# Optimization experiments

Hardware: AMD Instinct MI355X
Metric: run time of the kernel (lower is better)

The kernel has to match this reference:

```python
import jax, jax.numpy as jnp
import numpy as np

N_NODES = 2708      # hardcoded in GCN.__init__ (DictLearn(2708, nfeat/2))
NFEAT = 4096
M_DICT = NFEAT // 2 # dictionary atoms
NHID = 1024
NCLASS = 64
POWER_ITER = 100
FISTA_ITER = 20


def power_method(W, key):
    # nm -> largest eigenvalue of W^T W (sigma_max(W)^2)
    X0 = jax.random.normal(key, (1, W.shape[1]), dtype=W.dtype)
    def body(i, carry):
        X, _ = carry
        Xn = (X @ W.T) @ W
        nm = jnp.linalg.norm(Xn)
        return (Xn / nm, nm)
    _, nm = jax.lax.fori_loop(0, POWER_ITER, body, (X0, jnp.float32(1.0)))
    return nm


def soft_threshold(X, lam):
    return jnp.sign(X) * jax.nn.relu(jnp.abs(X) - lam)


def fista(Y, W, lam, key):
    # torch sets W.requires_grad_(False) during sparse coding
    Ws = jax.lax.stop_gradient(W)
    c = power_method(Ws, key)
    eta = 1.0 / c
    Gamma0 = soft_threshold((eta * Ws).T @ Y, lam)   # (m, nfeat)
    Ynorm = jnp.linalg.norm(Y)
    def step(carry, _):
        Gamma, Z, t = carry
        residual = Ws @ Z - Y                         # (n, nfeat)
        Gamma_new = soft_threshold(Z - eta * (Ws.T @ residual), lam / c)
        t_new = (1.0 + jnp.sqrt(1.0 + 4.0 * t * t)) / 2.0
        Z_new = Gamma_new + (t - 1.0) / t_new * (Gamma_new - Gamma)
        nrm = jnp.linalg.norm(residual) / Ynorm
        return (Gamma_new, Z_new, t_new), nrm
    (Gamma, _, _), norms = jax.lax.scan(
        step, (Gamma0, Gamma0, jnp.float32(1.0)), None, length=FISTA_ITER)
    return Gamma, norms


def setup_inputs() -> dict:
    key = jax.random.key(0)
    ks = jax.random.split(key, 7)
    x = jax.random.normal(ks[0], (N_NODES, NFEAT), dtype=jnp.float32)
    # dense stand-in for the normalized sparse adjacency; scaled to keep activations sane
    adj = jax.random.uniform(ks[1], (N_NODES, N_NODES), dtype=jnp.float32) / N_NODES
    stdv1 = 1.0 / np.sqrt(NHID)
    gc1_w = jax.random.uniform(ks[2], (NFEAT, NHID), minval=-stdv1, maxval=stdv1, dtype=jnp.float32)
    gc1_b = jax.random.uniform(ks[3], (NHID,), minval=-stdv1, maxval=stdv1, dtype=jnp.float32)
    stdv2 = 1.0 / np.sqrt(NCLASS)
    gc2_w = jax.random.uniform(ks[4], (NHID, NCLASS), minval=-stdv2, maxval=stdv2, dtype=jnp.float32)
    gc2_b = jax.random.uniform(ks[5], (NCLASS,), minval=-stdv2, maxval=stdv2, dtype=jnp.float32)
    # torch normalizes W in-place via .data, so the learnable leaf IS the normalized dict
    W_dict = jax.random.normal(ks[6], (N_NODES, M_DICT), dtype=jnp.float32)
    W_dict = W_dict / jnp.linalg.norm(W_dict, axis=0, keepdims=True)
    return {"x": x, "adj": adj, "gc1_w": gc1_w, "gc1_b": gc1_b,
            "gc2_w": gc2_w, "gc2_b": gc2_b, "W_dict": W_dict, "K": 1}


def reference(x, adj, gc1_w, gc1_b, gc2_w, gc2_b, W_dict, K):
    # SC='fista' (the only dimensionally consistent path); K acts as lamda
    lam = jnp.float32(K)
    Gamma, norms = fista(x, W_dict, lam, jax.random.key(1))  # (m, nfeat)
    x_dec = W_dict @ Gamma                                   # (n, nfeat)
    h = jax.nn.relu(adj @ (x_dec @ gc1_w) + gc1_b)           # dropout is identity in eval
    out = adj @ (h @ gc2_w) + gc2_b
    return jax.nn.log_softmax(out, axis=1), x_dec, Gamma, norms
```

## Files before the change

### kernel.cpp

```cpp
#include <hip/hip_runtime.h>
#include <cstdint>
#include <cmath>

#define NN_ 2708
#define NF_ 4096
#define MD_ 2048
#define NH_ 1024
#define NC_ 64
#define FITER 20
#define KPAD 2720


typedef _Float16 half8_t __attribute__((ext_vector_type(8)));
typedef _Float16 half4_t __attribute__((ext_vector_type(4)));
typedef float floatx4_t __attribute__((ext_vector_type(4)));

__device__ __forceinline__ float softt(float v, float t) {
    float a = fabsf(v) - t;
    a = a > 0.f ? a : 0.f;
    return copysignf(a, v);
}

__device__ __forceinline__ float blockReduceSum(float v, float* red) {
    int lane = threadIdx.x & 63, wid = threadIdx.x >> 6;
    #pragma unroll
    for (int off = 32; off; off >>= 1) v += __shfl_down(v, off);
    if (lane == 0) red[wid] = v;
    __syncthreads();
    if (wid == 0) {
        int nw = (blockDim.x + 63) >> 6;
        float r = (lane < nw) ? red[lane] : 0.f;
        #pragma unroll
        for (int off = 4; off; off >>= 1) r += __shfl_down(r, off);
        if (lane == 0) red[0] = r;
    }
    __syncthreads();
    float out = red[0];
    __syncthreads();
    return out;
}

__device__ __forceinline__ float erfinv_f(float x) {
    float w = -log1pf(-x * x);
    float p;
    if (w < 5.0f) {
        w -= 2.5f;
        p = 2.81022636e-08f;
        p = fmaf(p, w, 3.43273939e-07f);
        p = fmaf(p, w, -3.5233877e-06f);
        p = fmaf(p, w, -4.39150654e-06f);
        p = fmaf(p, w, 0.00021858087f);
        p = fmaf(p, w, -0.00125372503f);
        p = fmaf(p, w, -0.00417768164f);
        p = fmaf(p, w, 0.246640727f);
        p = fmaf(p, w, 1.50140941f);
    } else {
        w = sqrtf(w) - 3.0f;
        p = -0.000200214257f;
        p = fmaf(p, w, 0.000100950558f);
        p = fmaf(p, w, 0.00134934322f);
        p = fmaf(p, w, -0.00367342844f);
        p = fmaf(p, w, 0.00573950773f);
        p = fmaf(p, w, -0.0076224613f);
        p = fmaf(p, w, 0.00943887047f);
        p = fmaf(p, w, 1.00167406f);
        p = fmaf(p, w, 2.83297682f);
    }
    return p * x;
}

__device__ __forceinline__ float u32_to_normal(uint32_t bits) {
    uint32_t fb = (bits >> 9) | 0x3F800000u;
    float f = __uint_as_float(fb) - 1.0f;
    const float lo = -0.99999994f;
    float u = fmaf(f, 2.0f, lo);
    u = fmaxf(lo, u);
    return 1.41421356f * erfinv_f(u);
}

__global__ void init_x0_kernel(float* __restrict__ X0) {
    int i = blockIdx.x * blockDim.x + threadIdx.x;
    if (i >= MD_ / 2) return;
    uint32_t x0 = (uint32_t)i, x1 = (uint32_t)(i + MD_ / 2);
    const uint32_t k0 = 0u, k1 = 1u, k2 = 0x1BD11BDBu;
    const uint32_t ks[3] = {k0, k1, k2};
    x0 += k0; x1 += k1;
    const int rot[8] = {13, 15, 26, 6, 17, 29, 16, 24};
    #pragma unroll
    for (int g = 0; g < 5; ++g) {
        const int base = (g & 1) ? 4 : 0;
        #pragma unroll
        for (int rr = 0; rr < 4; ++rr) {
            x0 += x1;
            int r = rot[base + rr];
            x1 = (x1 << r) | (x1 >> (32 - r));
            x1 ^= x0;
        }
        x0 += ks[(g + 1) % 3];
        x1 += ks[(g + 2) % 3] + (uint32_t)(g + 1);
    }
    X0[i] = u32_to_normal(x0);
    X0[i + MD_ / 2] = u32_to_normal(x1);
}

__global__ void zero_scal_kernel(float* __restrict__ scal) {
    int t = threadIdx.x;
    if (t < 32) scal[t] = 0.f;
}

__global__ void fill0_kernel(uint32_t* __restrict__ p, int n32) {
    int i = blockIdx.x * blockDim.x + threadIdx.x;
    if (i < n32) p[i] = 0u;
}

__global__ void sumsq_kernel(const float* __restrict__ X, int n, float* __restrict__ acc) {
    __shared__ float red[8];
    float s = 0.f;
    for (size_t i = (size_t)blockIdx.x * blockDim.x + threadIdx.x; i < (size_t)n;
         i += (size_t)gridDim.x * blockDim.x) {
        float v = X[i];
        s += v * v;
    }
    s = blockReduceSum(s, red);
    if (threadIdx.x == 0) atomicAdd(acc, s);
}

__global__ void tsplit_kernel(const float* __restrict__ src, int R, int ld, int Rpad,
                              _Float16* __restrict__ hi, _Float16* __restrict__ lo) {
    __shared__ float t[32][33];
    int rb = blockIdx.y * 32, cb = blockIdx.x * 32;
    int tx = threadIdx.x & 31, ty = threadIdx.x >> 5;
    #pragma unroll
    for (int s = 0; s < 32; s += 8) {
        int r = rb + ty + s, c = cb + tx;
        t[ty + s][tx] = (r < R) ? src[(size_t)r * ld + c] : 0.f;
    }
    __syncthreads();
    #pragma unroll
    for (int s = 0; s < 32; s += 8) {
        int c = cb + ty + s, r = rb + tx;
        float v = t[tx][ty + s];
        _Float16 h = (_Float16)v;
        size_t o = (size_t)c * Rpad + r;
        hi[o] = h;
        lo[o] = (_Float16)(v - (float)h);
    }
}

__global__ void splitrows_hi_kernel(const float* __restrict__ src, int R, int C,
                                    _Float16* __restrict__ hi) {
    int r = blockIdx.x;
    _Float16* d = hi + (size_t)r * C;
    if (r < R) {
        const float* s = src + (size_t)r * C;
        for (int c = threadIdx.x * 4; c < C; c += 1024) {
            float4 v = *reinterpret_cast<const float4*>(s + c);
            half4_t h;
            h[0] = (_Float16)v.x; h[1] = (_Float16)v.y;
            h[2] = (_Float16)v.z; h[3] = (_Float16)v.w;
            *reinterpret_cast<half4_t*>(d + c) = h;
        }
    } else {
        for (int c = threadIdx.x * 4; c < C; c += 1024) {
            half4_t h = {(_Float16)0.f, (_Float16)0.f, (_Float16)0.f, (_Float16)0.f};
            *reinterpret_cast<half4_t*>(d + c) = h;
        }
    }
}

__global__ void splitadj_hi_kernel(const float* __restrict__ adj, _Float16* __restrict__ hi) {
    int r = blockIdx.x;
    bool rok = r < NN_;
    _Float16* d = hi + (size_t)r * KPAD;
    const float* s = adj + (size_t)r * NN_;
    for (int c = threadIdx.x * 4; c < KPAD; c += 1024) {
        half4_t h = {(_Float16)0.f, (_Float16)0.f, (_Float16)0.f, (_Float16)0.f};
        if (rok && c + 3 < NN_) {
            float4 v = *reinterpret_cast<const float4*>(s + c);
            h[0] = (_Float16)v.x; h[1] = (_Float16)v.y;
            h[2] = (_Float16)v.z; h[3] = (_Float16)v.w;
        }
        *reinterpret_cast<half4_t*>(d + c) = h;
    }
}

__global__ void g0_kernel(const float* __restrict__ Bm, const float* __restrict__ scal,
                          float* __restrict__ Gamma,
                          _Float16* __restrict__ Zh, _Float16* __restrict__ Zl) {
    __shared__ float t[32][33];
    int rb = blockIdx.y * 32;
    int cb = blockIdx.x * 32;
    float eta = scal[1], lam = scal[3];
    int tx = threadIdx.x & 31, ty = threadIdx.x >> 5;
    #pragma unroll
    for (int s = 0; s < 32; s += 8) {
        int r = rb + ty + s, c = cb + tx;
        float g = softt(eta * Bm[(size_t)r * NF_ + c], lam);
        Gamma[(size_t)r * NF_ + c] = g;
        t[ty + s][tx] = g;
    }
    __syncthreads();
    #pragma unroll
    for (int s = 0; s < 32; s += 8) {
        int c = cb + ty + s, r = rb + tx;
        float v = t[tx][ty + s];
        _Float16 h = (_Float16)v;
        size_t o = (size_t)c * MD_ + r;
        Zh[o] = h;
        Zl[o] = (_Float16)(v - (float)h);
    }
}

__global__ __launch_bounds__(256)
void papply_kernel(const _Float16* __restrict__ Mh, const _Float16* __restrict__ Ml,
                   const float* __restrict__ Xc, float* __restrict__ Xn, int addI) {
    __shared__ float xs[MD_];
    __shared__ float red[8];
    const int tid = threadIdx.x;
    float ss = 0.f;
    for (int k = tid; k < MD_; k += 256) { float v = Xc[k]; xs[k] = v; ss += v * v; }
    __syncthreads();
    ss = blockReduceSum(ss, red);
    float inv = 1.0f / sqrtf(ss);
    const int w = tid >> 6, l = tid & 63;
    const int r = blockIdx.x * 4 + w;
    const _Float16* mhr = Mh + (size_t)r * MD_;
    const _Float16* mlr = Ml + (size_t)r * MD_;
    float s = 0.f;
    #pragma unroll
    for (int q = 0; q < 8; ++q) {
        int o = (q * 64 + l) * 4;
        half4_t hv = *reinterpret_cast<const half4_t*>(mhr + o);
        half4_t lv = *reinterpret_cast<const half4_t*>(mlr + o);
        float4 xv = *reinterpret_cast<const float4*>(&xs[o]);
        s = fmaf((float)hv[0] + (float)lv[0], xv.x, s);
        s = fmaf((float)hv[1] + (float)lv[1], xv.y, s);
        s = fmaf((float)hv[2] + (float)lv[2], xv.z, s);
        s = fmaf((float)hv[3] + (float)lv[3], xv.w, s);
    }
    #pragma unroll
    for (int off = 32; off; off >>= 1) s += __shfl_down(s, off);
    if (l == 0) Xn[r] = (s + (addI ? xs[r] : 0.f)) * inv;
}

__global__ void pfinal_kernel(const float* __restrict__ Xf, const int* __restrict__ Kp,
                              float* __restrict__ scal) {
    __shared__ float red[8];
    float ss = 0.f;
    for (int k = threadIdx.x; k < MD_; k += 256) { float v = Xf[k]; ss += v * v; }
    ss = blockReduceSum(ss, red);
    if (threadIdx.x == 0) {
        float c = sqrtf(ss);
        float lam = (float)Kp[0];
        scal[0] = c;
        scal[1] = 1.0f / c;
        scal[2] = lam / c;
        scal[3] = lam;
    }
}

enum { ME_STORE = 0, ME_SYMSPLIT = 1, ME_SYMSPLIT_MI = 2, ME_H1 = 3, ME_SYMSPLIT16 = 4,
       ME_SPLIT_T = 5, ME_FISTAG = 6, ME_FISTAG_LAST = 7, ME_BIAS = 8, ME_BIASRELU = 9 };

__device__ __forceinline__ void stage_h(const _Float16* __restrict__ g, int row0, int K, int kk,
                                        _Float16* s, int tid) {
    const int row = tid >> 2;
    const int kg = (tid & 3) ^ ((row >> 1) & 3);
    const _Float16* gp = g + (size_t)(row0 + row) * K + kk + (kg << 3);
    _Float16* lp = s + ((size_t)((tid >> 6) * 64) << 3);
    __builtin_amdgcn_global_load_lds(
        (const __attribute__((address_space(1))) void*)gp,
        (__attribute__((address_space(3))) void*)lp, 16, 0, 0);
}

template <bool AFP32, bool THREE>
__global__ __launch_bounds__(512)
void mgemm_kernel(const _Float16* __restrict__ Ah, const _Float16* __restrict__ Al,
                  const float* __restrict__ Afp, int Marr,
                  const _Float16* __restrict__ Bh, const _Float16* __restrict__ Bl,
                  int K, int Mvalid, int Nvalid, int ldc,
                  float* __restrict__ C, const float* __restrict__ BmP,
                  const float* __restrict__ bias,
                  _Float16* __restrict__ Th, _Float16* __restrict__ Tl, int Tstride,
                  const float* __restrict__ scal, float betak,
                  float* __restrict__ nrm_acc, int epi) {
    constexpr int TILE = 128 * 32;
    constexpr int TPB = THREE ? 4 : 3;
    constexpr int NT = AFP32 ? 4 : 3 * TPB;
    __shared__ __align__(16) _Float16 smem[NT * TILE];
    float* red = (float*)smem;
    const int tid = threadIdx.x;
    const int w = tid >> 6, l = tid & 63;
    const int wr = w >> 2, wc = w & 3;
    const int quad = l >> 4, lc = l & 15;
    const int row0 = blockIdx.y * 128, col0 = blockIdx.x * 128;

    const int qs = (quad ^ ((lc >> 1) & 3)) << 3;

    floatx4_t acc[4][2];
    #pragma unroll
    for (int i = 0; i < 4; ++i)
        #pragma unroll
        for (int j = 0; j < 2; ++j) {
            floatx4_t z = {0.f, 0.f, 0.f, 0.f};
            acc[i][j] = z;
        }

    if constexpr (!AFP32) {
        const int NTK = K >> 5;
        auto STAGE = [&](int kt, int b) {
            _Float16* base = smem + b * (TPB * TILE);
            stage_h(Ah, row0, K, kt << 5, base, tid);
            if constexpr (THREE) stage_h(Al, row0, K, kt << 5, base + TILE, tid);
            stage_h(Bh, col0, K, kt << 5, base + (THREE ? 2 : 1) * TILE, tid);
            stage_h(Bl, col0, K, kt << 5, base + (THREE ? 3 : 2) * TILE, tid);
        };
        STAGE(0, 0);
        if (NTK > 1) {
            STAGE(1, 1);
            if constexpr (THREE) asm volatile("s_waitcnt vmcnt(4)" ::: "memory");
            else                 asm volatile("s_waitcnt vmcnt(3)" ::: "memory");
        } else {
            asm volatile("s_waitcnt vmcnt(0)" ::: "memory");
        }
        __builtin_amdgcn_s_barrier();
        for (int t = 0; t < NTK; ++t) {
            const int cur = t % 3;
            if (t + 2 < NTK) STAGE(t + 2, (t + 2) % 3);
            const _Float16* base = smem + cur * (TPB * TILE);
            const _Float16* pAh = base;
            const _Float16* pAl = base + TILE;
            const _Float16* pBh = base + (THREE ? 2 : 1) * TILE;
            const _Float16* pBl = base + (THREE ? 3 : 2) * TILE;
            half8_t fAh[4], fAl[4], fBh[2], fBl[2];
            #pragma unroll
            for (int i = 0; i < 4; ++i) {
                int oa = (wr * 64 + i * 16 + lc) * 32 + qs;
                fAh[i] = *reinterpret_cast<const half8_t*>(&pAh[oa]);
                if constexpr (THREE) fAl[i] = *reinterpret_cast<const half8_t*>(&pAl[oa]);
            }
            #pragma unroll
            for (int j = 0; j < 2; ++j) {
                int ob = (wc * 32 + j * 16 + lc) * 32 + qs;
                fBh[j] = *reinterpret_cast<const half8_t*>(&pBh[ob]);
                fBl[j] = *reinterpret_cast<const half8_t*>(&pBl[ob]);
            }
            #pragma unroll
            for (int i = 0; i < 4; ++i)
                #pragma unroll
                for (int j = 0; j < 2; ++j) {
                    acc[i][j] = __builtin_amdgcn_mfma_f32_16x16x32_f16(fAh[i], fBh[j], acc[i][j], 0, 0, 0);
                    acc[i][j] = __builtin_amdgcn_mfma_f32_16x16x32_f16(fAh[i], fBl[j], acc[i][j], 0, 0, 0);
                    if constexpr (THREE)
                        acc[i][j] = __builtin_amdgcn_mfma_f32_16x16x32_f16(fAl[i], fBh[j], acc[i][j], 0, 0, 0);
                }
            __builtin_amdgcn_sched_barrier(0);
            if (t + 2 < NTK) {
                if constexpr (THREE) asm volatile("s_waitcnt vmcnt(4)" ::: "memory");
                else                 asm volatile("s_waitcnt vmcnt(3)" ::: "memory");
            } else {
                asm volatile("s_waitcnt vmcnt(0)" ::: "memory");
            }
            __builtin_amdgcn_s_barrier();
        }
    } else {
        _Float16* sAh = smem;
        _Float16* sAl = smem + TILE;
        _Float16* sBh = smem + 2 * TILE;
        _Float16* sBl = smem + 3 * TILE;
        for (int kk = 0; kk < K; kk += 32) {
            #pragma unroll
            for (int p = 0; p < 2; ++p) {
                int c2 = p * 512 + tid;
                int r2 = c2 >> 3, k4 = (c2 & 7) << 2;
                int gr = row0 + r2;
                gr = gr < Marr ? gr : Marr - 1;
                float4 v = *reinterpret_cast<const float4*>(Afp + (size_t)gr * K + kk + k4);
                half4_t hh, ll;
                hh[0] = (_Float16)v.x; ll[0] = (_Float16)(v.x - (float)hh[0]);
                hh[1] = (_Float16)v.y; ll[1] = (_Float16)(v.y - (float)hh[1]);
                hh[2] = (_Float16)v.z; ll[2] = (_Float16)(v.z - (float)hh[2]);
                hh[3] = (_Float16)v.w; ll[3] = (_Float16)(v.w - (float)hh[3]);
                int sw = (((k4 >> 3) ^ ((r2 >> 1) & 3)) << 3) | (k4 & 7);
                *reinterpret_cast<half4_t*>(&sAh[r2 * 32 + sw]) = hh;
                *reinterpret_cast<half4_t*>(&sAl[r2 * 32 + sw]) = ll;
            }
            stage_h(Bh, col0, K, kk, sBh, tid);
            stage_h(Bl, col0, K, kk, sBl, tid);
            asm volatile("s_waitcnt vmcnt(0)" ::: "memory");
            __syncthreads();

            half8_t fAh[4], fAl[4], fBh[2], fBl[2];
            #pragma unroll
            for (int i = 0; i < 4; ++i) {
                int oa = (wr * 64 + i * 16 + lc) * 32 + qs;
                fAh[i] = *reinterpret_cast<const half8_t*>(&sAh[oa]);
                fAl[i] = *reinterpret_cast<const half8_t*>(&sAl[oa]);
            }
            #pragma unroll
            for (int j = 0; j < 2; ++j) {
                int ob = (wc * 32 + j * 16 + lc) * 32 + qs;
                fBh[j] = *reinterpret_cast<const half8_t*>(&sBh[ob]);
                fBl[j] = *reinterpret_cast<const half8_t*>(&sBl[ob]);
            }
            #pragma unroll
            for (int i = 0; i < 4; ++i)
                #pragma unroll
                for (int j = 0; j < 2; ++j) {
                    acc[i][j] = __builtin_amdgcn_mfma_f32_16x16x32_f16(fAh[i], fBh[j], acc[i][j], 0, 0, 0);
                    acc[i][j] = __builtin_amdgcn_mfma_f32_16x16x32_f16(fAh[i], fBl[j], acc[i][j], 0, 0, 0);
                    acc[i][j] = __builtin_amdgcn_mfma_f32_16x16x32_f16(fAl[i], fBh[j], acc[i][j], 0, 0, 0);
                }
            __syncthreads();
        }
    }

    float eta = 0.f, thr = 0.f;
    if (epi == ME_FISTAG || epi == ME_FISTAG_LAST) { eta = scal[1]; thr = scal[2]; }
    float rsq = 0.f;
    #pragma unroll
    for (int i = 0; i < 4; ++i) {
        int grow0 = row0 + wr * 64 + i * 16 + quad * 4;
        bool rowok = grow0 < Mvalid;
        #pragma unroll
        for (int j = 0; j < 2; ++j) {
            int gcol = col0 + wc * 32 + j * 16 + lc;
            bool colok = gcol < Nvalid;
            floatx4_t v = acc[i][j];
            if (epi == ME_STORE) {
                if (rowok && colok) {
                    #pragma unroll
                    for (int r2 = 0; r2 < 4; ++r2) C[(size_t)(grow0 + r2) * ldc + gcol] = v[r2];
                }
            } else if (epi == ME_SYMSPLIT || epi == ME_SYMSPLIT_MI || epi == ME_H1 ||
                       epi == ME_SYMSPLIT16) {
                #pragma unroll
                for (int r2 = 0; r2 < 4; ++r2) {
                    float vv = v[r2];
                    float dg = ((grow0 + r2) == gcol) ? 1.f : 0.f;
                    size_t o = (size_t)(grow0 + r2) * Tstride + gcol;
                    if (epi == ME_SYMSPLIT_MI) {
                        vv -= dg;
                    } else if (epi == ME_H1) {
                        float ev = (float)Ah[o] + (float)Al[o];
                        vv = (vv + 2.f * ev + dg) * 0.0625f;
                    } else if (epi == ME_SYMSPLIT16) {
                        vv *= 16.f;
                    }
                    _Float16 h = (_Float16)vv;
                    Th[o] = h;
                    Tl[o] = (_Float16)(vv - (float)h);
                }
            } else if (epi == ME_SPLIT_T) {
                if (rowok && colok) {
                    half4_t hh, ll;
                    #pragma unroll
                    for (int r2 = 0; r2 < 4; ++r2) {
                        _Float16 h = (_Float16)v[r2];
                        hh[r2] = h; ll[r2] = (_Float16)(v[r2] - (float)h);
                    }
                    size_t to = (size_t)gcol * Tstride + grow0;
                    *reinterpret_cast<half4_t*>(&Th[to]) = hh;
                    *reinterpret_cast<half4_t*>(&Tl[to]) = ll;
                }
            } else if (epi == ME_FISTAG || epi == ME_FISTAG_LAST) {
                size_t to = (size_t)gcol * Tstride + grow0;
                half4_t zh = *reinterpret_cast<const half4_t*>(&Bh[to]);
                half4_t zl = *reinterpret_cast<const half4_t*>(&Bl[to]);
                half4_t oh, ol;
                #pragma unroll
                for (int r2 = 0; r2 < 4; ++r2) {
                    float z = (float)zh[r2] + (float)zl[r2];
                    float p = v[r2] + z;
                    float bi = BmP[(size_t)(grow0 + r2) * NF_ + gcol];
                    rsq = fmaf(z, p - 2.0f * bi, rsq);
                    float g = z - eta * (p - bi);
                    float gn = softt(g, thr);
                    size_t ci = (size_t)(grow0 + r2) * NF_ + gcol;
                    float gold = C[ci];
                    C[ci] = gn;
                    float zo = (epi == ME_FISTAG) ? (gn + betak * (gn - gold)) : gn;
                    _Float16 h = (_Float16)zo;
                    oh[r2] = h; ol[r2] = (_Float16)(zo - (float)h);
                }
                *reinterpret_cast<half4_t*>(&Th[to]) = oh;
                *reinterpret_cast<half4_t*>(&Tl[to]) = ol;
            } else {
                if (rowok && colok) {
                    #pragma unroll
                    for (int r2 = 0; r2 < 4; ++r2) {
                        float s = v[r2] + bias[gcol];
                        if (epi == ME_BIASRELU) s = s > 0.f ? s : 0.f;
                        C[(size_t)(grow0 + r2) * ldc + gcol] = s;
                    }
                }
            }
        }
    }
    if (epi == ME_FISTAG || epi == ME_FISTAG_LAST) {
        float tot = blockReduceSum(rsq, red);
        if (tid == 0) atomicAdd(nrm_acc, tot);
    }
}

__global__ void logsoftmax_kernel(const float* __restrict__ O, float* __restrict__ out) {
    int row = blockIdx.x * 4 + (threadIdx.x >> 6);
    int lane = threadIdx.x & 63;
    if (row >= NN_) return;
    float v = O[row * NC_ + lane];
    float m = v;
    #pragma unroll
    for (int off = 32; off; off >>= 1) m = fmaxf(m, __shfl_xor(m, off));
    float e = expf(v - m);
    float s = e;
    #pragma unroll
    for (int off = 32; off; off >>= 1) s += __shfl_xor(s, off);
    out[row * NC_ + lane] = (v - m) - logf(s);
}

__global__ void norms_kernel(const float* __restrict__ scal, float* __restrict__ nout) {
    int k = threadIdx.x;
    if (k < FITER) {
        float ysq = scal[4];
        float v = scal[5 + k] + ysq;
        nout[k] = sqrtf(fmaxf(v, 0.f)) / sqrtf(ysq);
    }
}

static inline void launch_m(bool afp32, bool three, dim3 grid,
                            const _Float16* Ah, const _Float16* Al,
                            const float* Afp, int Marr,
                            const _Float16* Bh, const _Float16* Bl,
                            int K, int Mvalid, int Nvalid, int ldc,
                            float* C, const float* BmP, const float* bias,
                            _Float16* Th, _Float16* Tl, int Tstride,
                            const float* scal, float betak, float* nrm, int epi,
                            hipStream_t s) {
    if (afp32)
        mgemm_kernel<true, true><<<grid, dim3(512), 0, s>>>(
            Ah, Al, Afp, Marr, Bh, Bl, K, Mvalid, Nvalid, ldc, C, BmP, bias,
            Th, Tl, Tstride, scal, betak, nrm, epi);
    else if (three)
        mgemm_kernel<false, true><<<grid, dim3(512), 0, s>>>(
            Ah, Al, Afp, Marr, Bh, Bl, K, Mvalid, Nvalid, ldc, C, BmP, bias,
            Th, Tl, Tstride, scal, betak, nrm, epi);
    else
        mgemm_kernel<false, false><<<grid, dim3(512), 0, s>>>(
            Ah, Al, Afp, Marr, Bh, Bl, K, Mvalid, Nvalid, ldc, C, BmP, bias,
            Th, Tl, Tstride, scal, betak, nrm, epi);
}

extern "C" void kernel_launch(void* const* d_in, const int* in_sizes, int n_in,
                              void* d_out, int out_size, void* d_ws, size_t ws_size,
                              hipStream_t stream) {
    const float* x     = (const float*)d_in[0];
    const float* adj   = (const float*)d_in[1];
    const float* gc1_w = (const float*)d_in[2];
    const float* gc1_b = (const float*)d_in[3];
    const float* gc2_w = (const float*)d_in[4];
    const float* gc2_b = (const float*)d_in[5];
    const float* Wd    = (const float*)d_in[6];
    const int*   Kp    = (const int*)d_in[7];

    float* out = (float*)d_out;
    float* logp    = out;
    float* x_dec   = logp + (size_t)NN_ * NC_;
    float* Gamma   = x_dec + (size_t)NN_ * NF_;
    float* norms_o = Gamma + (size_t)MD_ * NF_;

    char* wsb = (char*)d_ws;
    const size_t OFF_R1 = 16512;
    const size_t OFF_R2 = OFF_R1 + 16777216;
    const size_t OFF_R3 = OFF_R2 + 33554432;
    const size_t OFF_R4 = OFF_R3 + 33554432;
    float* scal = (float*)wsb;
    float* Xa   = scal + 32;
    float* Xb   = Xa + MD_;
    _Float16* Eh = (_Float16*)(wsb + OFF_R1);
    _Float16* El = Eh + (size_t)MD_ * MD_;
    float* Bm = (float*)(wsb + OFF_R2);
    _Float16* Wt_hi  = (_Float16*)(wsb + OFF_R3);
    _Float16* Wt_lo  = Wt_hi + (size_t)MD_ * KPAD;
    _Float16* xth_hi = Wt_lo + (size_t)MD_ * KPAD;
    _Float16* xth_lo = (_Float16*)(wsb + OFF_R4);
    _Float16* HA_hi = (_Float16*)(wsb + OFF_R4);
    _Float16* HA_lo = HA_hi + (size_t)MD_ * MD_;
    _Float16* HB_hi = (_Float16*)(wsb + OFF_R3);
    _Float16* HB_lo = HB_hi + (size_t)MD_ * MD_;
    _Float16* ZA_hi = (_Float16*)(wsb + OFF_R3);
    _Float16* ZA_lo = ZA_hi + (size_t)NF_ * MD_;
    _Float16* ZB_hi = (_Float16*)x_dec;
    _Float16* ZB_lo = ZB_hi + (size_t)NF_ * MD_;
    _Float16* adjT_hi = (_Float16*)(wsb + OFF_R2);
    _Float16* xwT_hi  = (_Float16*)(wsb + OFF_R2 + 15319040);
    _Float16* xwT_lo  = xwT_hi + (size_t)NH_ * KPAD;
    _Float16* g1t_hi  = (_Float16*)(wsb + OFF_R1);
    _Float16* g1t_lo  = g1t_hi + (size_t)NH_ * NF_;
    _Float16* xdh     = (_Float16*)(wsb + OFF_R3);
    float*    hbuf    = (float*)(wsb + OFF_R3);
    _Float16* Wh      = (_Float16*)(wsb + OFF_R4);
    _Float16* g2t_hi  = (_Float16*)(wsb + OFF_R4 + 11534336);
    _Float16* g2t_lo  = g2t_hi + (size_t)128 * NH_;
    _Float16* hwT_hi  = (_Float16*)(wsb + OFF_R4 + 12058624);
    _Float16* hwT_lo  = hwT_hi + (size_t)128 * KPAD;
    float*    obuf    = (float*)(wsb + OFF_R4 + 13451264);

    const _Float16* nullh = nullptr;
    float* nullf = nullptr;

    zero_scal_kernel<<<1, 64, 0, stream>>>(scal);
    init_x0_kernel<<<4, 256, 0, stream>>>(Xa);
    sumsq_kernel<<<1024, 256, 0, stream>>>(x, NN_ * NF_, scal + 4);

    tsplit_kernel<<<dim3(MD_ / 32, KPAD / 32), 256, 0, stream>>>(Wd, NN_, MD_, KPAD, Wt_hi, Wt_lo);
    launch_m(false, true, dim3(16, 16), Wt_hi, Wt_lo, nullptr, 0, Wt_hi, Wt_lo,
             KPAD, MD_, MD_, 0, nullf, nullptr, nullptr, Eh, El, MD_,
             scal, 0.f, nullptr, ME_SYMSPLIT_MI, stream);
    for (int half = 0; half < 2; ++half) {
        tsplit_kernel<<<dim3(MD_ / 32, KPAD / 32), 256, 0, stream>>>(
            x + half * 2048, NN_, NF_, KPAD, xth_hi, xth_lo);
        launch_m(false, false, dim3(16, 16), Wt_hi, Wt_lo, nullptr, 0, xth_hi, xth_lo,
                 KPAD, MD_, MD_, NF_, Bm + half * 2048, nullptr, nullptr,
                 nullptr, nullptr, 0, scal, 0.f, nullptr, ME_STORE, stream);
    }
    launch_m(false, false, dim3(16, 16), Eh, El, nullptr, 0, Eh, El,
             MD_, MD_, MD_, 0, nullf, nullptr, nullptr, HA_hi, HA_lo, MD_,
             scal, 0.f, nullptr, ME_H1, stream);
    launch_m(false, false, dim3(16, 16), HA_hi, HA_lo, nullptr, 0, HA_hi, HA_lo,
             MD_, MD_, MD_, 0, nullf, nullptr, nullptr, HB_hi, HB_lo, MD_,
             scal, 0.f, nullptr, ME_SYMSPLIT, stream);
    launch_m(false, false, dim3(16, 16), HB_hi, HB_lo, nullptr, 0, HB_hi, HB_lo,
             MD_, MD_, MD_, 0, nullf, nullptr, nullptr, HA_hi, HA_lo, MD_,
             scal, 0.f, nullptr, ME_SYMSPLIT, stream);
    launch_m(false, false, dim3(16, 16), HA_hi, HA_lo, nullptr, 0, HA_hi, HA_lo,
             MD_, MD_, MD_, 0, nullf, nullptr, nullptr, HB_hi, HB_lo, MD_,
             scal, 0.f, nullptr, ME_SYMSPLIT, stream);
    launch_m(false, false, dim3(16, 16), HB_hi, HB_lo, nullptr, 0, HB_hi, HB_lo,
             MD_, MD_, MD_, 0, nullf, nullptr, nullptr, HA_hi, HA_lo, MD_,
             scal, 0.f, nullptr, ME_SYMSPLIT16, stream);
    for (int it = 0; it < 7; ++it) {
        const _Float16* mh = (it < 3) ? HA_hi : Eh;
        const _Float16* ml = (it < 3) ? HA_lo : El;
        const float* xin = (it & 1) ? Xb : Xa;
        float* xout = (it & 1) ? Xa : Xb;
        papply_kernel<<<MD_ / 4, 256, 0, stream>>>(mh, ml, xin, xout, (it >= 3) ? 1 : 0);
    }
    pfinal_kernel<<<1, 256, 0, stream>>>(Xb, Kp, scal);
    g0_kernel<<<dim3(NF_ / 32, MD_ / 32), 256, 0, stream>>>(Bm, scal, Gamma, ZA_hi, ZA_lo);

    {
        float t = 1.f;
        for (int k = 0; k < FITER; ++k) {
            float tn = (1.0f + sqrtf(1.0f + (4.0f * t) * t)) / 2.0f;
            float beta = (t - 1.0f) / tn;
            t = tn;
            _Float16* in_hi  = (k & 1) ? ZB_hi : ZA_hi;
            _Float16* in_lo  = (k & 1) ? ZB_lo : ZA_lo;
            _Float16* out_hi = (k & 1) ? ZA_hi : ZB_hi;
            _Float16* out_lo = (k & 1) ? ZA_lo : ZB_lo;
            launch_m(false, false, dim3(32, 16), Eh, El, nullptr, 0, in_hi, in_lo,
                     MD_, MD_, NF_, NF_, Gamma, Bm, nullptr,
                     out_hi, out_lo, MD_, scal, beta, scal + 5 + k,
                     (k == FITER - 1) ? ME_FISTAG_LAST : ME_FISTAG, stream);
        }
    }

    splitadj_hi_kernel<<<2816, 256, 0, stream>>>(adj, adjT_hi);
    splitrows_hi_kernel<<<2816, 256, 0, stream>>>(Wd, NN_, MD_, Wh);
    launch_m(false, false, dim3(32, 22), Wh, Wh, nullptr, 0, ZA_hi, ZA_lo,
             MD_, NN_, NF_, NF_, x_dec, nullptr, nullptr,
             nullptr, nullptr, 0, scal, 0.f, nullptr, ME_STORE, stream);
    splitrows_hi_kernel<<<2816, 256, 0, stream>>>(x_dec, NN_, NF_, xdh);
    tsplit_kernel<<<dim3(NH_ / 32, NF_ / 32), 256, 0, stream>>>(gc1_w, NF_, NH_, NF_, g1t_hi, g1t_lo);
    fill0_kernel<<<(2785280 + 255) / 256, 256, 0, stream>>>((uint32_t*)xwT_hi, 2785280);
    launch_m(false, false, dim3(8, 22), xdh, xdh, nullptr, 0, g1t_hi, g1t_lo,
             NF_, NN_, NH_, 0, nullf, nullptr, nullptr,
             xwT_hi, xwT_lo, KPAD, scal, 0.f, nullptr, ME_SPLIT_T, stream);
    launch_m(false, false, dim3(8, 22), adjT_hi, adjT_hi, nullptr, 0, xwT_hi, xwT_lo,
             KPAD, NN_, NH_, NH_, hbuf, nullptr, gc1_b,
             nullptr, nullptr, 0, scal, 0.f, nullptr, ME_BIASRELU, stream);
    fill0_kernel<<<(131072 + 255) / 256, 256, 0, stream>>>((uint32_t*)g2t_hi, 131072);
    tsplit_kernel<<<dim3(NC_ / 32, NH_ / 32), 256, 0, stream>>>(gc2_w, NH_, NC_, NH_, g2t_hi, g2t_lo);
    fill0_kernel<<<(348160 + 255) / 256, 256, 0, stream>>>((uint32_t*)hwT_hi, 348160);
    launch_m(true, true, dim3(1, 22), nullh, nullh, hbuf, NN_, g2t_hi, g2t_lo,
             NH_, NN_, NC_, 0, nullf, nullptr, nullptr,
             hwT_hi, hwT_lo, KPAD, scal, 0.f, nullptr, ME_SPLIT_T, stream);
    launch_m(false, false, dim3(1, 22), adjT_hi, adjT_hi, nullptr, 0, hwT_hi, hwT_lo,
             KPAD, NN_, NC_, NC_, obuf, nullptr, gc2_b,
             nullptr, nullptr, 0, scal, 0.f, nullptr, ME_BIAS, stream);
    logsoftmax_kernel<<<(NN_ + 3) / 4, 256, 0, stream>>>(obuf, logp);
    norms_kernel<<<1, 32, 0, stream>>>(scal, norms_o);
}
```

Measured before the change: 2.949 ms.

## Transpose FISTA state layout so epilogue accesses are row-contiguous with new AHL GEMM mode

Adds a GEMM mode that splits the A operand into hi/lo halves instead of B, with a 32x64 warp tile. The FISTA iteration now computes the transposed product (Z^T E), so Gamma, Bm and Z are kept in transposed, feature-major layout. This makes the epilogue reads and writes of Gamma, Bm and Z follow the GEMM output rows, and lets the initial soft-threshold kernel become a plain vectorized elementwise pass. The last iteration writes Gamma back in the original layout through a strided scalar store. The epilogue now uses scalar fp16 loads and stores, and the warp tile shape changes register and LDS read balance.

```diff
diff --git a/kernel.cpp b/kernel.cpp
--- a/kernel.cpp
+++ b/kernel.cpp
@@ -184,31 +184,25 @@
     }
 }
 
-__global__ void g0_kernel(const float* __restrict__ Bm, const float* __restrict__ scal,
-                          float* __restrict__ Gamma,
+__global__ void g0_kernel(const float* __restrict__ BmT, const float* __restrict__ scal,
+                          float* __restrict__ GammaT,
                           _Float16* __restrict__ Zh, _Float16* __restrict__ Zl) {
-    __shared__ float t[32][33];
-    int rb = blockIdx.y * 32;
-    int cb = blockIdx.x * 32;
     float eta = scal[1], lam = scal[3];
-    int tx = threadIdx.x & 31, ty = threadIdx.x >> 5;
-    #pragma unroll
-    for (int s = 0; s < 32; s += 8) {
-        int r = rb + ty + s, c = cb + tx;
-        float g = softt(eta * Bm[(size_t)r * NF_ + c], lam);
-        Gamma[(size_t)r * NF_ + c] = g;
-        t[ty + s][tx] = g;
-    }
-    __syncthreads();
-    #pragma unroll
-    for (int s = 0; s < 32; s += 8) {
-        int c = cb + ty + s, r = rb + tx;
-        float v = t[tx][ty + s];
-        _Float16 h = (_Float16)v;
-        size_t o = (size_t)c * MD_ + r;
-        Zh[o] = h;
-        Zl[o] = (_Float16)(v - (float)h);
-    }
+    size_t i = ((size_t)blockIdx.x * blockDim.x + threadIdx.x) * 4;
+    float4 b = *reinterpret_cast<const float4*>(BmT + i);
+    float4 g;
+    g.x = softt(eta * b.x, lam);
+    g.y = softt(eta * b.y, lam);
+    g.z = softt(eta * b.z, lam);
+    g.w = softt(eta * b.w, lam);
+    *reinterpret_cast<float4*>(GammaT + i) = g;
+    half4_t hh, ll;
+    hh[0] = (_Float16)g.x; ll[0] = (_Float16)(g.x - (float)hh[0]);
+    hh[1] = (_Float16)g.y; ll[1] = (_Float16)(g.y - (float)hh[1]);
+    hh[2] = (_Float16)g.z; ll[2] = (_Float16)(g.z - (float)hh[2]);
+    hh[3] = (_Float16)g.w; ll[3] = (_Float16)(g.w - (float)hh[3]);
+    *reinterpret_cast<half4_t*>(Zh + i) = hh;
+    *reinterpret_cast<half4_t*>(Zl + i) = ll;
 }
 
 __global__ __launch_bounds__(256)
@@ -261,6 +255,7 @@
 
 enum { ME_STORE = 0, ME_SYMSPLIT = 1, ME_SYMSPLIT_MI = 2, ME_H1 = 3, ME_SYMSPLIT16 = 4,
        ME_SPLIT_T = 5, ME_FISTAG = 6, ME_FISTAG_LAST = 7, ME_BIAS = 8, ME_BIASRELU = 9 };
+enum { MO_BHL = 0, MO_AHL = 1, MO_THREE = 2, MO_AFP32 = 3 };
 
 __device__ __forceinline__ void stage_h(const _Float16* __restrict__ g, int row0, int K, int kk,
                                         _Float16* s, int tid) {
@@ -273,7 +268,7 @@
         (__attribute__((address_space(3))) void*)lp, 16, 0, 0);
 }
 
-template <bool AFP32, bool THREE>
+template <int MODE>
 __global__ __launch_bounds__(512)
 void mgemm_kernel(const _Float16* __restrict__ Ah, const _Float16* __restrict__ Al,
                   const float* __restrict__ Afp, int Marr,
@@ -285,41 +280,47 @@
                   const float* __restrict__ scal, float betak,
                   float* __restrict__ nrm_acc, int epi) {
     constexpr int TILE = 128 * 32;
-    constexpr int TPB = THREE ? 4 : 3;
-    constexpr int NT = AFP32 ? 4 : 3 * TPB;
+    constexpr int TPB = (MODE == MO_THREE) ? 4 : 3;
+    constexpr int NT = (MODE == MO_AFP32) ? 4 : 3 * TPB;
+    constexpr bool A4 = (MODE == MO_AHL);
+    constexpr int WTR = A4 ? 32 : 64, WTC = A4 ? 64 : 32;
+    constexpr int AI = WTR / 16, BJ = WTC / 16;
+    constexpr int BOFF = (MODE == MO_BHL) ? 1 : 2;
     __shared__ __align__(16) _Float16 smem[NT * TILE];
     float* red = (float*)smem;
     const int tid = threadIdx.x;
     const int w = tid >> 6, l = tid & 63;
-    const int wr = w >> 2, wc = w & 3;
+    const int wr = A4 ? (w >> 1) : (w >> 2);
+    const int wc = A4 ? (w & 1) : (w & 3);
     const int quad = l >> 4, lc = l & 15;
     const int row0 = blockIdx.y * 128, col0 = blockIdx.x * 128;
-
     const int qs = (quad ^ ((lc >> 1) & 3)) << 3;
 
-    floatx4_t acc[4][2];
-    #pragma unroll
-    for (int i = 0; i < 4; ++i)
+    floatx4_t acc[AI][BJ];
+    #pragma unroll
+    for (int i = 0; i < AI; ++i)
         #pragma unroll
-        for (int j = 0; j < 2; ++j) {
+        for (int j = 0; j < BJ; ++j) {
             floatx4_t z = {0.f, 0.f, 0.f, 0.f};
             acc[i][j] = z;
         }
 
-    if constexpr (!AFP32) {
+    if constexpr (MODE != MO_AFP32) {
         const int NTK = K >> 5;
         auto STAGE = [&](int kt, int b) {
             _Float16* base = smem + b * (TPB * TILE);
             stage_h(Ah, row0, K, kt << 5, base, tid);
-            if constexpr (THREE) stage_h(Al, row0, K, kt << 5, base + TILE, tid);
-            stage_h(Bh, col0, K, kt << 5, base + (THREE ? 2 : 1) * TILE, tid);
-            stage_h(Bl, col0, K, kt << 5, base + (THREE ? 3 : 2) * TILE, tid);
+            if constexpr (MODE == MO_AHL || MODE == MO_THREE)
+                stage_h(Al, row0, K, kt << 5, base + TILE, tid);
+            stage_h(Bh, col0, K, kt << 5, base + BOFF * TILE, tid);
+            if constexpr (MODE == MO_BHL || MODE == MO_THREE)
+                stage_h(Bl, col0, K, kt << 5, base + (BOFF + 1) * TILE, tid);
         };
         STAGE(0, 0);
         if (NTK > 1) {
             STAGE(1, 1);
-            if constexpr (THREE) asm volatile("s_waitcnt vmcnt(4)" ::: "memory");
-            else                 asm volatile("s_waitcnt vmcnt(3)" ::: "memory");
+            if constexpr (TPB == 4) asm volatile("s_waitcnt vmcnt(4)" ::: "memory");
+            else                    asm volatile("s_waitcnt vmcnt(3)" ::: "memory");
         } else {
             asm volatile("s_waitcnt vmcnt(0)" ::: "memory");
         }
@@ -330,34 +331,37 @@
             const _Float16* base = smem + cur * (TPB * TILE);
             const _Float16* pAh = base;
             const _Float16* pAl = base + TILE;
-            const _Float16* pBh = base + (THREE ? 2 : 1) * TILE;
-            const _Float16* pBl = base + (THREE ? 3 : 2) * TILE;
-            half8_t fAh[4], fAl[4], fBh[2], fBl[2];
+            const _Float16* pBh = base + BOFF * TILE;
+            const _Float16* pBl = base + (BOFF + 1) * TILE;
+            half8_t fAh[AI], fAl[AI], fBh[BJ], fBl[BJ];
             #pragma unroll
-            for (int i = 0; i < 4; ++i) {
-                int oa = (wr * 64 + i * 16 + lc) * 32 + qs;
+            for (int i = 0; i < AI; ++i) {
+                int oa = (wr * WTR + i * 16 + lc) * 32 + qs;
                 fAh[i] = *reinterpret_cast<const half8_t*>(&pAh[oa]);
-                if constexpr (THREE) fAl[i] = *reinterpret_cast<const half8_t*>(&pAl[oa]);
+                if constexpr (MODE == MO_AHL || MODE == MO_THREE)
+                    fAl[i] = *reinterpret_cast<const half8_t*>(&pAl[oa]);
             }
             #pragma unroll
-            for (int j = 0; j < 2; ++j) {
-                int ob = (wc * 32 + j * 16 + lc) * 32 + qs;
+            for (int j = 0; j < BJ; ++j) {
+                int ob = (wc * WTC + j * 16 + lc) * 32 + qs;
                 fBh[j] = *reinterpret_cast<const half8_t*>(&pBh[ob]);
-                fBl[j] = *reinterpret_cast<const half8_t*>(&pBl[ob]);
+                if constexpr (MODE == MO_BHL || MODE == MO_THREE)
+                    fBl[j] = *reinterpret_cast<const half8_t*>(&pBl[ob]);
             }
             #pragma unroll
-            for (int i = 0; i < 4; ++i)
+            for (int i = 0; i < AI; ++i)
                 #pragma unroll
-                for (int j = 0; j < 2; ++j) {
+                for (int j = 0; j < BJ; ++j) {
                     acc[i][j] = __builtin_amdgcn_mfma_f32_16x16x32_f16(fAh[i], fBh[j], acc[i][j], 0, 0, 0);
-                    acc[i][j] = __builtin_amdgcn_mfma_f32_16x16x32_f16(fAh[i], fBl[j], acc[i][j], 0, 0, 0);
-                    if constexpr (THREE)
+                    if constexpr (MODE == MO_BHL || MODE == MO_THREE)
+                        acc[i][j] = __builtin_amdgcn_mfma_f32_16x16x32_f16(fAh[i], fBl[j], acc[i][j], 0, 0, 0);
+                    if constexpr (MODE == MO_AHL || MODE == MO_THREE)
                         acc[i][j] = __builtin_amdgcn_mfma_f32_16x16x32_f16(fAl[i], fBh[j], acc[i][j], 0, 0, 0);
                 }
             __builtin_amdgcn_sched_barrier(0);
             if (t + 2 < NTK) {
-                if constexpr (THREE) asm volatile("s_waitcnt vmcnt(4)" ::: "memory");
-                else                 asm volatile("s_waitcnt vmcnt(3)" ::: "memory");
+                if constexpr (TPB == 4) asm volatile("s_waitcnt vmcnt(4)" ::: "memory");
+                else                    asm volatile("s_waitcnt vmcnt(3)" ::: "memory");
             } else {
                 asm volatile("s_waitcnt vmcnt(0)" ::: "memory");
             }
@@ -390,23 +394,23 @@
             asm volatile("s_waitcnt vmcnt(0)" ::: "memory");
             __syncthreads();
 
-            half8_t fAh[4], fAl[4], fBh[2], fBl[2];
+            half8_t fAh[AI], fAl[AI], fBh[BJ], fBl[BJ];
             #pragma unroll
-            for (int i = 0; i < 4; ++i) {
-                int oa = (wr * 64 + i * 16 + lc) * 32 + qs;
+            for (int i = 0; i < AI; ++i) {
+                int oa = (wr * WTR + i * 16 + lc) * 32 + qs;
                 fAh[i] = *reinterpret_cast<const half8_t*>(&sAh[oa]);
                 fAl[i] = *reinterpret_cast<const half8_t*>(&sAl[oa]);
             }
             #pragma unroll
-            for (int j = 0; j < 2; ++j) {
-                int ob = (wc * 32 + j * 16 + lc) * 32 + qs;
+            for (int j = 0; j < BJ; ++j) {
+                int ob = (wc * WTC + j * 16 + lc) * 32 + qs;
                 fBh[j] = *reinterpret_cast<const half8_t*>(&sBh[ob]);
                 fBl[j] = *reinterpret_cast<const half8_t*>(&sBl[ob]);
             }
             #pragma unroll
-            for (int i = 0; i < 4; ++i)
+            for (int i = 0; i < AI; ++i)
                 #pragma unroll
-                for (int j = 0; j < 2; ++j) {
+                for (int j = 0; j < BJ; ++j) {
                     acc[i][j] = __builtin_amdgcn_mfma_f32_16x16x32_f16(fAh[i], fBh[j], acc[i][j], 0, 0, 0);
                     acc[i][j] = __builtin_amdgcn_mfma_f32_16x16x32_f16(fAh[i], fBl[j], acc[i][j], 0, 0, 0);
                     acc[i][j] = __builtin_amdgcn_mfma_f32_16x16x32_f16(fAl[i], fBh[j], acc[i][j], 0, 0, 0);
@@ -419,12 +423,12 @@
     if (epi == ME_FISTAG || epi == ME_FISTAG_LAST) { eta = scal[1]; thr = scal[2]; }
     float rsq = 0.f;
     #pragma unroll
-    for (int i = 0; i < 4; ++i) {
-        int grow0 = row0 + wr * 64 + i * 16 + quad * 4;
+    for (int i = 0; i < AI; ++i) {
+        int grow0 = row0 + wr * WTR + i * 16 + quad * 4;
         bool rowok = grow0 < Mvalid;
         #pragma unroll
-        for (int j = 0; j < 2; ++j) {
-            int gcol = col0 + wc * 32 + j * 16 + lc;
+        for (int j = 0; j < BJ; ++j) {
+            int gcol = col0 + wc * WTC + j * 16 + lc;
             bool colok = gcol < Nvalid;
             floatx4_t v = acc[i][j];
             if (epi == ME_STORE) {
@@ -464,27 +468,28 @@
                     *reinterpret_cast<half4_t*>(&Tl[to]) = ll;
                 }
             } else if (epi == ME_FISTAG || epi == ME_FISTAG_LAST) {
-                size_t to = (size_t)gcol * Tstride + grow0;
-                half4_t zh = *reinterpret_cast<const half4_t*>(&Bh[to]);
-                half4_t zl = *reinterpret_cast<const half4_t*>(&Bl[to]);
-                half4_t oh, ol;
                 #pragma unroll
                 for (int r2 = 0; r2 < 4; ++r2) {
-                    float z = (float)zh[r2] + (float)zl[r2];
+                    size_t idx = (size_t)(grow0 + r2) * (size_t)Tstride + gcol;
+                    float z = (float)Ah[idx] + (float)Al[idx];
                     float p = v[r2] + z;
-                    float bi = BmP[(size_t)(grow0 + r2) * NF_ + gcol];
+                    float bi = BmP[idx];
                     rsq = fmaf(z, p - 2.0f * bi, rsq);
                     float g = z - eta * (p - bi);
                     float gn = softt(g, thr);
-                    size_t ci = (size_t)(grow0 + r2) * NF_ + gcol;
-                    float gold = C[ci];
-                    C[ci] = gn;
-                    float zo = (epi == ME_FISTAG) ? (gn + betak * (gn - gold)) : gn;
+                    float zo;
+                    if (epi == ME_FISTAG) {
+                        float gold = C[idx];
+                        C[idx] = gn;
+                        zo = gn + betak * (gn - gold);
+                    } else {
+                        C[(size_t)gcol * NF_ + (grow0 + r2)] = gn;
+                        zo = gn;
+                    }
                     _Float16 h = (_Float16)zo;
-                    oh[r2] = h; ol[r2] = (_Float16)(zo - (float)h);
+                    Th[idx] = h;
+                    Tl[idx] = (_Float16)(zo - (float)h);
                 }
-                *reinterpret_cast<half4_t*>(&Th[to]) = oh;
-                *reinterpret_cast<half4_t*>(&Tl[to]) = ol;
             } else {
                 if (rowok && colok) {
                     #pragma unroll
@@ -527,7 +532,7 @@
     }
 }
 
-static inline void launch_m(bool afp32, bool three, dim3 grid,
+static inline void launch_m(int mode, dim3 grid,
                             const _Float16* Ah, const _Float16* Al,
                             const float* Afp, int Marr,
                             const _Float16* Bh, const _Float16* Bl,
@@ -536,18 +541,28 @@
                             _Float16* Th, _Float16* Tl, int Tstride,
                             const float* scal, float betak, float* nrm, int epi,
                             hipStream_t s) {
-    if (afp32)
-        mgemm_kernel<true, true><<<grid, dim3(512), 0, s>>>(
+    switch (mode) {
+    case MO_BHL:
+        mgemm_kernel<MO_BHL><<<grid, dim3(512), 0, s>>>(
             Ah, Al, Afp, Marr, Bh, Bl, K, Mvalid, Nvalid, ldc, C, BmP, bias,
             Th, Tl, Tstride, scal, betak, nrm, epi);
-    else if (three)
-        mgemm_kernel<false, true><<<grid, dim3(512), 0, s>>>(
+        break;
+    case MO_AHL:
+        mgemm_kernel<MO_AHL><<<grid, dim3(512), 0, s>>>(
             Ah, Al, Afp, Marr, Bh, Bl, K, Mvalid, Nvalid, ldc, C, BmP, bias,
             Th, Tl, Tstride, scal, betak, nrm, epi);
-    else
-        mgemm_kernel<false, false><<<grid, dim3(512), 0, s>>>(
+        break;
+    case MO_THREE:
+        mgemm_kernel<MO_THREE><<<grid, dim3(512), 0, s>>>(
             Ah, Al, Afp, Marr, Bh, Bl, K, Mvalid, Nvalid, ldc, C, BmP, bias,
             Th, Tl, Tstride, scal, betak, nrm, epi);
+        break;
+    default:
+        mgemm_kernel<MO_AFP32><<<grid, dim3(512), 0, s>>>(
+            Ah, Al, Afp, Marr, Bh, Bl, K, Mvalid, Nvalid, ldc, C, BmP, bias,
+            Th, Tl, Tstride, scal, betak, nrm, epi);
+        break;
+    }
 }
 
 extern "C" void kernel_launch(void* const* d_in, const int* in_sizes, int n_in,
@@ -567,6 +582,7 @@
     float* x_dec   = logp + (size_t)NN_ * NC_;
     float* Gamma   = x_dec + (size_t)NN_ * NF_;
     float* norms_o = Gamma + (size_t)MD_ * NF_;
+    float* GammaT = Gamma;
 
     char* wsb = (char*)d_ws;
     const size_t OFF_R1 = 16512;
@@ -578,7 +594,7 @@
     float* Xb   = Xa + MD_;
     _Float16* Eh = (_Float16*)(wsb + OFF_R1);
     _Float16* El = Eh + (size_t)MD_ * MD_;
-    float* Bm = (float*)(wsb + OFF_R2);
+    float* BmT = (float*)(wsb + OFF_R2);
     _Float16* Wt_hi  = (_Float16*)(wsb + OFF_R3);
     _Float16* Wt_lo  = Wt_hi + (size_t)MD_ * KPAD;
     _Float16* xth_hi = Wt_lo + (size_t)MD_ * KPAD;
@@ -613,29 +629,29 @@
     sumsq_kernel<<<1024, 256, 0, stream>>>(x, NN_ * NF_, scal + 4);
 
     tsplit_kernel<<<dim3(MD_ / 32, KPAD / 32), 256, 0, stream>>>(Wd, NN_, MD_, KPAD, Wt_hi, Wt_lo);
-    launch_m(false, true, dim3(16, 16), Wt_hi, Wt_lo, nullptr, 0, Wt_hi, Wt_lo,
+    launch_m(MO_THREE, dim3(16, 16), Wt_hi, Wt_lo, nullptr, 0, Wt_hi, Wt_lo,
              KPAD, MD_, MD_, 0, nullf, nullptr, nullptr, Eh, El, MD_,
              scal, 0.f, nullptr, ME_SYMSPLIT_MI, stream);
     for (int half = 0; half < 2; ++half) {
         tsplit_kernel<<<dim3(MD_ / 32, KPAD / 32), 256, 0, stream>>>(
             x + half * 2048, NN_, NF_, KPAD, xth_hi, xth_lo);
-        launch_m(false, false, dim3(16, 16), Wt_hi, Wt_lo, nullptr, 0, xth_hi, xth_lo,
-                 KPAD, MD_, MD_, NF_, Bm + half * 2048, nullptr, nullptr,
+        launch_m(MO_AHL, dim3(16, 16), xth_hi, xth_lo, nullptr, 0, Wt_hi, Wt_lo,
+                 KPAD, 2048, MD_, MD_, BmT + (size_t)half * 2048 * MD_, nullptr, nullptr,
                  nullptr, nullptr, 0, scal, 0.f, nullptr, ME_STORE, stream);
     }
-    launch_m(false, false, dim3(16, 16), Eh, El, nullptr, 0, Eh, El,
+    launch_m(MO_BHL, dim3(16, 16), Eh, El, nullptr, 0, Eh, El,
              MD_, MD_, MD_, 0, nullf, nullptr, nullptr, HA_hi, HA_lo, MD_,
              scal, 0.f, nullptr, ME_H1, stream);
-    launch_m(false, false, dim3(16, 16), HA_hi, HA_lo, nullptr, 0, HA_hi, HA_lo,
+    launch_m(MO_BHL, dim3(16, 16), HA_hi, HA_lo, nullptr, 0, HA_hi, HA_lo,
              MD_, MD_, MD_, 0, nullf, nullptr, nullptr, HB_hi, HB_lo, MD_,
              scal, 0.f, nullptr, ME_SYMSPLIT, stream);
-    launch_m(false, false, dim3(16, 16), HB_hi, HB_lo, nullptr, 0, HB_hi, HB_lo,
+    launch_m(MO_BHL, dim3(16, 16), HB_hi, HB_lo, nullptr, 0, HB_hi, HB_lo,
              MD_, MD_, MD_, 0, nullf, nullptr, nullptr, HA_hi, HA_lo, MD_,
              scal, 0.f, nullptr, ME_SYMSPLIT, stream);
-    launch_m(false, false, dim3(16, 16), HA_hi, HA_lo, nullptr, 0, HA_hi, HA_lo,
+    launch_m(MO_BHL, dim3(16, 16), HA_hi, HA_lo, nullptr, 0, HA_hi, HA_lo,
              MD_, MD_, MD_, 0, nullf, nullptr, nullptr, HB_hi, HB_lo, MD_,
              scal, 0.f, nullptr, ME_SYMSPLIT, stream);
-    launch_m(false, false, dim3(16, 16), HB_hi, HB_lo, nullptr, 0, HB_hi, HB_lo,
+    launch_m(MO_BHL, dim3(16, 16), HB_hi, HB_lo, nullptr, 0, HB_hi, HB_lo,
              MD_, MD_, MD_, 0, nullf, nullptr, nullptr, HA_hi, HA_lo, MD_,
              scal, 0.f, nullptr, ME_SYMSPLIT16, stream);
     for (int it = 0; it < 7; ++it) {
@@ -646,7 +662,7 @@
         papply_kernel<<<MD_ / 4, 256, 0, stream>>>(mh, ml, xin, xout, (it >= 3) ? 1 : 0);
     }
     pfinal_kernel<<<1, 256, 0, stream>>>(Xb, Kp, scal);
-    g0_kernel<<<dim3(NF_ / 32, MD_ / 32), 256, 0, stream>>>(Bm, scal, Gamma, ZA_hi, ZA_lo);
+    g0_kernel<<<(NF_ * MD_ / 4) / 256, 256, 0, stream>>>(BmT, scal, GammaT, ZA_hi, ZA_lo);
 
     {
         float t = 1.f;
@@ -658,8 +674,8 @@
             _Float16* in_lo  = (k & 1) ? ZB_lo : ZA_lo;
             _Float16* out_hi = (k & 1) ? ZA_hi : ZB_hi;
             _Float16* out_lo = (k & 1) ? ZA_lo : ZB_lo;
-            launch_m(false, false, dim3(32, 16), Eh, El, nullptr, 0, in_hi, in_lo,
-                     MD_, MD_, NF_, NF_, Gamma, Bm, nullptr,
+            launch_m(MO_AHL, dim3(MD_ / 128, NF_ / 128), in_hi, in_lo, nullptr, 0, Eh, El,
+                     MD_, NF_, MD_, NF_, GammaT, BmT, nullptr,
                      out_hi, out_lo, MD_, scal, beta, scal + 5 + k,
                      (k == FITER - 1) ? ME_FISTAG_LAST : ME_FISTAG, stream);
         }
@@ -667,25 +683,25 @@
 
     splitadj_hi_kernel<<<2816, 256, 0, stream>>>(adj, adjT_hi);
     splitrows_hi_kernel<<<2816, 256, 0, stream>>>(Wd, NN_, MD_, Wh);
-    launch_m(false, false, dim3(32, 22), Wh, Wh, nullptr, 0, ZA_hi, ZA_lo,
+    launch_m(MO_BHL, dim3(32, 22), Wh, Wh, nullptr, 0, ZA_hi, ZA_lo,
              MD_, NN_, NF_, NF_, x_dec, nullptr, nullptr,
              nullptr, nullptr, 0, scal, 0.f, nullptr, ME_STORE, stream);
     splitrows_hi_kernel<<<2816, 256, 0, stream>>>(x_dec, NN_, NF_, xdh);
     tsplit_kernel<<<dim3(NH_ / 32, NF_ / 32), 256, 0, stream>>>(gc1_w, NF_, NH_, NF_, g1t_hi, g1t_lo);
     fill0_kernel<<<(2785280 + 255) / 256, 256, 0, stream>>>((uint32_t*)xwT_hi, 2785280);
-    launch_m(false, false, dim3(8, 22), xdh, xdh, nullptr, 0, g1t_hi, g1t_lo,
+    launch_m(MO_BHL, dim3(8, 22), xdh, xdh, nullptr, 0, g1t_hi, g1t_lo,
              NF_, NN_, NH_, 0, nullf, nullptr, nullptr,
              xwT_hi, xwT_lo, KPAD, scal, 0.f, nullptr, ME_SPLIT_T, stream);
-    launch_m(false, false, dim3(8, 22), adjT_hi, adjT_hi, nullptr, 0, xwT_hi, xwT_lo,
+    launch_m(MO_BHL, dim3(8, 22), adjT_hi, adjT_hi, nullptr, 0, xwT_hi, xwT_lo,
              KPAD, NN_, NH_, NH_, hbuf, nullptr, gc1_b,
              nullptr, nullptr, 0, scal, 0.f, nullptr, ME_BIASRELU, stream);
     fill0_kernel<<<(131072 + 255) / 256, 256, 0, stream>>>((uint32_t*)g2t_hi, 131072);
     tsplit_kernel<<<dim3(NC_ / 32, NH_ / 32), 256, 0, stream>>>(gc2_w, NH_, NC_, NH_, g2t_hi, g2t_lo);
     fill0_kernel<<<(348160 + 255) / 256, 256, 0, stream>>>((uint32_t*)hwT_hi, 348160);
-    launch_m(true, true, dim3(1, 22), nullh, nullh, hbuf, NN_, g2t_hi, g2t_lo,
+    launch_m(MO_AFP32, dim3(1, 22), nullh, nullh, hbuf, NN_, g2t_hi, g2t_lo,
              NH_, NN_, NC_, 0, nullf, nullptr, nullptr,
              hwT_hi, hwT_lo, KPAD, scal, 0.f, nullptr, ME_SPLIT_T, stream);
-    launch_m(false, false, dim3(1, 22), adjT_hi, adjT_hi, nullptr, 0, hwT_hi, hwT_lo,
+    launch_m(MO_BHL, dim3(1, 22), adjT_hi, adjT_hi, nullptr, 0, hwT_hi, hwT_lo,
              KPAD, NN_, NC_, NC_, obuf, nullptr, gc2_b,
              nullptr, nullptr, 0, scal, 0.f, nullptr, ME_BIAS, stream);
     logsoftmax_kernel<<<(NN_ + 3) / 4, 256, 0, stream>>>(obuf, logp);
```

After: 3.081 ms. +4.5%, slower.

## Load A fragments directly from global into registers, stage only B in LDS

Applied to the files above, without the earlier changes.

The f16 split-precision GEMM now reads its A operand (hi and lo parts) straight from global memory into per-lane MFMA fragments, with no LDS staging. Only the B tiles stay in the triple-buffered global_load_lds pipeline, which shrinks shared memory from 9-12 tiles to 6 and lowers the vmcnt waits. The aim is less LDS traffic and footprint, possibly allowing higher occupancy. The cost is uncoalesced, strided global loads for A that are issued synchronously inside the k-loop and are not prefetched. Also, the A loads are counted by vmcnt, so the vmcnt(2) accounting may stall on them.

```diff
diff --git a/kernel.cpp b/kernel.cpp
--- a/kernel.cpp
+++ b/kernel.cpp
@@ -285,8 +285,7 @@
                   const float* __restrict__ scal, float betak,
                   float* __restrict__ nrm_acc, int epi) {
     constexpr int TILE = 128 * 32;
-    constexpr int TPB = THREE ? 4 : 3;
-    constexpr int NT = AFP32 ? 4 : 3 * TPB;
+    constexpr int NT = AFP32 ? 4 : 6;
     __shared__ __align__(16) _Float16 smem[NT * TILE];
     float* red = (float*)smem;
     const int tid = threadIdx.x;
@@ -308,37 +307,36 @@
 
     if constexpr (!AFP32) {
         const int NTK = K >> 5;
+        const _Float16* aBase = Ah + (size_t)(row0 + wr * 64 + lc) * K + quad * 8;
+        const _Float16* aBaseL = Al + (size_t)(row0 + wr * 64 + lc) * K + quad * 8;
         auto STAGE = [&](int kt, int b) {
-            _Float16* base = smem + b * (TPB * TILE);
-            stage_h(Ah, row0, K, kt << 5, base, tid);
-            if constexpr (THREE) stage_h(Al, row0, K, kt << 5, base + TILE, tid);
-            stage_h(Bh, col0, K, kt << 5, base + (THREE ? 2 : 1) * TILE, tid);
-            stage_h(Bl, col0, K, kt << 5, base + (THREE ? 3 : 2) * TILE, tid);
+            _Float16* base = smem + b * (2 * TILE);
+            stage_h(Bh, col0, K, kt << 5, base, tid);
+            stage_h(Bl, col0, K, kt << 5, base + TILE, tid);
         };
         STAGE(0, 0);
         if (NTK > 1) {
             STAGE(1, 1);
-            if constexpr (THREE) asm volatile("s_waitcnt vmcnt(4)" ::: "memory");
-            else                 asm volatile("s_waitcnt vmcnt(3)" ::: "memory");
+            asm volatile("s_waitcnt vmcnt(2)" ::: "memory");
         } else {
             asm volatile("s_waitcnt vmcnt(0)" ::: "memory");
         }
         __builtin_amdgcn_s_barrier();
         for (int t = 0; t < NTK; ++t) {
             const int cur = t % 3;
-            if (t + 2 < NTK) STAGE(t + 2, (t + 2) % 3);
-            const _Float16* base = smem + cur * (TPB * TILE);
-            const _Float16* pAh = base;
-            const _Float16* pAl = base + TILE;
-            const _Float16* pBh = base + (THREE ? 2 : 1) * TILE;
-            const _Float16* pBl = base + (THREE ? 3 : 2) * TILE;
-            half8_t fAh[4], fAl[4], fBh[2], fBl[2];
+            half8_t fAh[4], fAl[4];
             #pragma unroll
             for (int i = 0; i < 4; ++i) {
-                int oa = (wr * 64 + i * 16 + lc) * 32 + qs;
-                fAh[i] = *reinterpret_cast<const half8_t*>(&pAh[oa]);
-                if constexpr (THREE) fAl[i] = *reinterpret_cast<const half8_t*>(&pAl[oa]);
+                fAh[i] = *reinterpret_cast<const half8_t*>(aBase + (size_t)i * 16 * K + (t << 5));
+                if constexpr (THREE)
+                    fAl[i] = *reinterpret_cast<const half8_t*>(aBaseL + (size_t)i * 16 * K + (t << 5));
             }
+            __builtin_amdgcn_sched_barrier(0);
+            if (t + 2 < NTK) STAGE(t + 2, (t + 2) % 3);
+            const _Float16* base = smem + cur * (2 * TILE);
+            const _Float16* pBh = base;
+            const _Float16* pBl = base + TILE;
+            half8_t fBh[2], fBl[2];
             #pragma unroll
             for (int j = 0; j < 2; ++j) {
                 int ob = (wc * 32 + j * 16 + lc) * 32 + qs;
@@ -356,8 +354,7 @@
                 }
             __builtin_amdgcn_sched_barrier(0);
             if (t + 2 < NTK) {
-                if constexpr (THREE) asm volatile("s_waitcnt vmcnt(4)" ::: "memory");
-                else                 asm volatile("s_waitcnt vmcnt(3)" ::: "memory");
+                asm volatile("s_waitcnt vmcnt(2)" ::: "memory");
             } else {
                 asm volatile("s_waitcnt vmcnt(0)" ::: "memory");
             }
```

New measurement: 5.232 ms. 1.77x slower.
